# Performance work log

Measured on AMD Instinct MI355X. Metric: run time of the kernel, lower is better.

Reference implementation:

```python
import jax, jax.numpy as jnp
import numpy as np

B, F, V, E = 65536, 39, 100000, 16
EPS = 1e-5

def setup_inputs() -> dict:
    key = jax.random.key(0)
    ks = jax.random.split(key, 10)
    return {
        'Xi': jax.random.randint(ks[0], (B, F, 1), 0, V, dtype=jnp.int64) if jax.config.read('jax_enable_x64') else jax.random.randint(ks[0], (B, F, 1), 0, V, dtype=jnp.int32),
        'Xv': jax.random.uniform(ks[1], (B, F), dtype=jnp.float32),
        'emb1': jax.random.normal(ks[2], (F, V, 1), dtype=jnp.float32),
        'emb2': jax.random.normal(ks[3], (F, V, E), dtype=jnp.float32),
        'W1': jax.random.normal(ks[4], (F * E, 512), dtype=jnp.float32) * 0.02,
        'b1': jax.random.normal(ks[5], (512,), dtype=jnp.float32) * 0.02,
        'g1': jnp.ones((512,), jnp.float32),
        'be1': jnp.zeros((512,), jnp.float32),
        'W2': jax.random.normal(ks[6], (512, 256), dtype=jnp.float32) * 0.02,
        'b2': jax.random.normal(ks[7], (256,), dtype=jnp.float32) * 0.02,
        'g2': jnp.ones((256,), jnp.float32),
        'be2': jnp.zeros((256,), jnp.float32),
        'bias': jax.random.normal(ks[8], (1,), dtype=jnp.float32),
    }

def _batchnorm(x, g, b):
    mu = jnp.mean(x, axis=0)
    var = jnp.mean(jnp.square(x - mu), axis=0)  # biased var, torch BN training mode
    return (x - mu) * jax.lax.rsqrt(var + EPS) * g + b

def reference(Xi, Xv, emb1, emb2, W1, b1, g1, be1, W2, b2, g2, be2, bias):
    idx = Xi[:, :, 0]                                # [B, F]
    fidx = jnp.arange(F)[None, :]                    # [1, F]
    # fused per-field gathers: [B, F] and [B, F, E]
    first = emb1[fidx, idx, 0] * Xv                  # first-order, [B, F]
    fm2 = emb2[fidx, idx] * Xv[:, :, None]           # second-order embeds, [B, F, E]
    sum_emb = jnp.sum(fm2, axis=1)                   # [B, E]
    second = 0.5 * (jnp.square(sum_emb) - jnp.sum(jnp.square(fm2), axis=1))  # [B, E]
    # deep part (note: original forward never applies the final num_classes layer)
    deep = fm2.reshape(B, F * E)
    deep = _batchnorm(deep @ W1 + b1, g1, be1)
    deep = _batchnorm(deep @ W2 + b2, g2, be2)
    return bias + jnp.sum(first, axis=1) + jnp.sum(second, axis=1) + jnp.sum(deep, axis=1)
```

## Files before the change

kernel.cpp:

```cpp
#include <hip/hip_runtime.h>

#define B_ROWS 65536
#define F_FEAT 39
#define V_VOC  100000
#define D_PAD  640
#define BN_EPS 1e-5f
#define NPAIR  (39 * 32)

typedef __bf16 bf16x8 __attribute__((ext_vector_type(8)));
typedef float  f32x16 __attribute__((ext_vector_type(16)));

__device__ __forceinline__ unsigned short toBF(float x) {
  unsigned int u = __float_as_uint(x);
  u += 0x7fffu + ((u >> 16) & 1u);
  return (unsigned short)(u >> 16);
}

__global__ __launch_bounds__(256) void k0_prep(
    const int* __restrict__ Xi, const float* __restrict__ Xv,
    int* __restrict__ XiT, float* __restrict__ XvT,
    float* __restrict__ M, unsigned short* __restrict__ XT) {
  for (int i = threadIdx.x; i < 800; i += 256)
    M[(size_t)blockIdx.x * 800 + i] = 0.f;

  const int b0 = blockIdx.x * 128;
  for (int u = threadIdx.x; u < 16 * 128; u += 256) {
    int m = 624 + (u >> 7), j = u & 127;
    XT[(size_t)m * B_ROWS + b0 + j] = (m == 624) ? (unsigned short)0x3f80 : (unsigned short)0;
  }

  __shared__ int   ti[128][41];
  __shared__ float tv[128][41];
  for (int u = threadIdx.x; u < 128 * 39; u += 256) {
    int r = u / 39, f = u - r * 39;
    ti[r][f] = Xi[(size_t)b0 * 39 + u];
    tv[r][f] = Xv[(size_t)b0 * 39 + u];
  }
  __syncthreads();
  for (int u = threadIdx.x; u < 39 * 128; u += 256) {
    int f = u >> 7, j = u & 127;
    XiT[(size_t)f * B_ROWS + b0 + j] = ti[j][f];
    XvT[(size_t)f * B_ROWS + b0 + j] = tv[j][f];
  }
}

__global__ __launch_bounds__(1024) void k1f_gather(
    const int* __restrict__ XiT, const float* __restrict__ XvT,
    const float* __restrict__ emb1, const float* __restrict__ emb2,
    unsigned short* __restrict__ XT, float* __restrict__ FS1) {
  __shared__ unsigned short xs[2][16][264];

  const int seg = threadIdx.x & 3;
  const int bi  = threadIdx.x >> 2;
  const int dim = threadIdx.x >> 6;
  const int prt = threadIdx.x & 63;

  for (int idx = blockIdx.x; idx < NPAIR; idx += gridDim.x) {
    const int f = idx >> 5;
    const int c = idx & 31;
    const int b0 = c * 2048;
    const float* ef  = emb2 + (size_t)f * V_VOC * 16;
    const float* e1f = emb1 + (size_t)f * V_VOC;
    const int*   xi  = XiT + (size_t)f * B_ROWS + b0;
    const float* xv  = XvT + (size_t)f * B_ROWS + b0;
    unsigned short* xtBase = XT + (size_t)(f * 16) * B_ROWS + b0;
    float* fs1 = FS1 + (size_t)f * B_ROWS + b0;

    int   idA = xi[bi],        idB = xi[256 + bi];
    float xvA = xv[bi],        xvB = xv[256 + bi];
    float4 v = *reinterpret_cast<const float4*>(ef + (size_t)idA * 16 + seg * 4);

    for (int s = 0; s < 8; ++s) {
      const float4 cur = v;
      const float  xvc = xvA;
      const int    idc = idA;
      idA = idB; xvA = xvB;
      if (s + 2 < 8) {
        idB = xi[(s + 2) * 256 + bi];
        xvB = xv[(s + 2) * 256 + bi];
      }
      if (s + 1 < 8)
        v = *reinterpret_cast<const float4*>(ef + (size_t)idA * 16 + seg * 4);

      if (seg == 0) fs1[s * 256 + bi] = e1f[idc] * xvc;

      const int bf = s & 1;
      xs[bf][seg * 4 + 0][bi] = toBF(cur.x * xvc);
      xs[bf][seg * 4 + 1][bi] = toBF(cur.y * xvc);
      xs[bf][seg * 4 + 2][bi] = toBF(cur.z * xvc);
      xs[bf][seg * 4 + 3][bi] = toBF(cur.w * xvc);
      __syncthreads();
      uint2 w = *reinterpret_cast<const uint2*>(&xs[bf][dim][prt * 4]);
      *reinterpret_cast<uint2*>(xtBase + (size_t)dim * B_ROWS + s * 256 + prt * 4) = w;
    }
    __syncthreads();
  }
}

#define KSPLIT 64
__global__ __launch_bounds__(256) void k2_syrk(const unsigned short* __restrict__ XT,
                                               float* __restrict__ M) {
  const int p = blockIdx.x;
  const int xcd = p & 7;
  const int ks = ((p >> 3) / 15) * 8 + xcd;
  int pair = (p >> 3) % 15;
  int ti = 0;
  while (pair >= 5 - ti) { pair -= 5 - ti; ++ti; }
  const int tj = ti + pair;

  __shared__ unsigned short pa[128 * 64];
  __shared__ unsigned short pb[128 * 64];

  const int lane = threadIdx.x & 63, wid = threadIdx.x >> 6;
  const int wm = wid >> 1, wn = wid & 1;
  const int rl = lane & 31, hh = lane >> 5;

  f32x16 acc00, acc01, acc10, acc11;
#pragma unroll
  for (int i = 0; i < 16; ++i) { acc00[i] = 0.f; acc01[i] = 0.f; acc10[i] = 0.f; acc11[i] = 0.f; }

  const int krange = B_ROWS / KSPLIT;
  const int kbase = ks * krange;

  for (int kt = 0; kt < krange; kt += 64) {
    const int k0 = kbase + kt;
#pragma unroll
    for (int g2 = 0; g2 < 4; ++g2) {
      const int g = threadIdx.x + g2 * 256;
      const int r = g >> 3, j = g & 7;
      uint4 va = *reinterpret_cast<const uint4*>(XT + (size_t)(ti * 128 + r) * B_ROWS + k0 + j * 8);
      *reinterpret_cast<uint4*>((char*)pa + r * 128 + ((j ^ (r & 7)) << 4)) = va;
      uint4 vb = *reinterpret_cast<const uint4*>(XT + (size_t)(tj * 128 + r) * B_ROWS + k0 + j * 8);
      *reinterpret_cast<uint4*>((char*)pb + r * 128 + ((j ^ (r & 7)) << 4)) = vb;
    }
    __syncthreads();
#pragma unroll
    for (int kc = 0; kc < 4; ++kc) {
      const int ra0 = wm * 64 + rl, ra1 = wm * 64 + 32 + rl;
      const int rb0 = wn * 64 + rl, rb1 = wn * 64 + 32 + rl;
      bf16x8 a0 = *reinterpret_cast<const bf16x8*>((char*)pa + ra0 * 128 + (((kc * 2 + hh) ^ (ra0 & 7)) << 4));
      bf16x8 a1 = *reinterpret_cast<const bf16x8*>((char*)pa + ra1 * 128 + (((kc * 2 + hh) ^ (ra1 & 7)) << 4));
      bf16x8 b0 = *reinterpret_cast<const bf16x8*>((char*)pb + rb0 * 128 + (((kc * 2 + hh) ^ (rb0 & 7)) << 4));
      bf16x8 b1 = *reinterpret_cast<const bf16x8*>((char*)pb + rb1 * 128 + (((kc * 2 + hh) ^ (rb1 & 7)) << 4));
      acc00 = __builtin_amdgcn_mfma_f32_32x32x16_bf16(a0, b0, acc00, 0, 0, 0);
      acc01 = __builtin_amdgcn_mfma_f32_32x32x16_bf16(a0, b1, acc01, 0, 0, 0);
      acc10 = __builtin_amdgcn_mfma_f32_32x32x16_bf16(a1, b0, acc10, 0, 0, 0);
      acc11 = __builtin_amdgcn_mfma_f32_32x32x16_bf16(a1, b1, acc11, 0, 0, 0);
    }
    __syncthreads();
  }

#pragma unroll
  for (int rr = 0; rr < 16; ++rr) {
    const int rloc = (rr & 3) + ((rr >> 2) << 3) + hh * 4;
    const int row0 = ti * 128 + wm * 64 + rloc;
    const int row1 = row0 + 32;
    const int col0 = tj * 128 + wn * 64 + rl;
    atomicAdd(&M[row0 * D_PAD + col0], acc00[rr]);
    atomicAdd(&M[row0 * D_PAD + col0 + 32], acc01[rr]);
    atomicAdd(&M[row1 * D_PAD + col0], acc10[rr]);
    atomicAdd(&M[row1 * D_PAD + col0 + 32], acc11[rr]);
  }
}

__device__ __forceinline__ float fetchM(const float* M, int a, int b) {
  if ((a >> 7) > (b >> 7)) { int t = a; a = b; b = t; }
  return M[a * D_PAD + b];
}
__global__ void k3a_cov(const float* __restrict__ M, float* __restrict__ Cov,
                        float* __restrict__ mu) {
  const int i = blockIdx.x;
  const float inv = 1.f / 65536.f;
  const float mui = fetchM(M, 624, i) * inv;
  for (int j = threadIdx.x; j < D_PAD; j += 256) {
    float muj = fetchM(M, 624, j) * inv;
    Cov[i * D_PAD + j] = fetchM(M, i, j) * inv - mui * muj;
    if (i == 0) mu[j] = muj;
  }
}

__global__ __launch_bounds__(256) void qform(const float* __restrict__ Cov,
                                             const float* __restrict__ W, const int ldw,
                                             const float* __restrict__ g,
                                             float* __restrict__ alpha) {
  const int k0 = blockIdx.x * 2;
  __shared__ float w0s[624], w1s[624];
  for (int i = threadIdx.x; i < 624; i += 256) {
    w0s[i] = W[(size_t)i * ldw + k0];
    w1s[i] = W[(size_t)i * ldw + k0 + 1];
  }
  __syncthreads();
  const int j0 = threadIdx.x, j1 = threadIdx.x + 256, j2 = threadIdx.x + 512;
  const bool v2 = (j2 < 624);
  const float wj00 = w0s[j0], wj01 = w0s[j1], wj02 = v2 ? w0s[j2] : 0.f;
  const float wj10 = w1s[j0], wj11 = w1s[j1], wj12 = v2 ? w1s[j2] : 0.f;
  float acc0 = 0.f, acc1 = 0.f;
  for (int i = 0; i < 624; ++i) {
    const float wi0 = w0s[i], wi1 = w1s[i];
    const float* row = Cov + i * D_PAD;
    const float c0 = row[j0], c1 = row[j1], c2 = v2 ? row[j2] : 0.f;
    acc0 += wi0 * (c0 * wj00 + c1 * wj01 + c2 * wj02);
    acc1 += wi1 * (c0 * wj10 + c1 * wj11 + c2 * wj12);
  }
#pragma unroll
  for (int off = 32; off > 0; off >>= 1) {
    acc0 += __shfl_down(acc0, off);
    acc1 += __shfl_down(acc1, off);
  }
  __shared__ float pr[2][4];
  const int lane = threadIdx.x & 63, wv = threadIdx.x >> 6;
  if (lane == 0) { pr[0][wv] = acc0; pr[1][wv] = acc1; }
  __syncthreads();
  if (threadIdx.x == 0) {
    float v0 = pr[0][0] + pr[0][1] + pr[0][2] + pr[0][3];
    float v1 = pr[1][0] + pr[1][1] + pr[1][2] + pr[1][3];
    alpha[k0]     = g[k0]     * rsqrtf(v0 + BN_EPS);
    alpha[k0 + 1] = g[k0 + 1] * rsqrtf(v1 + BN_EPS);
  }
}

__global__ __launch_bounds__(256) void k3c_G(const float* __restrict__ W1,
                                             const float* __restrict__ alpha1,
                                             const float* __restrict__ W2,
                                             float* __restrict__ G) {
  const int i = blockIdx.x;
  __shared__ float a[512];
  for (int k = threadIdx.x; k < 512; k += 256)
    a[k] = W1[(size_t)i * 512 + k] * alpha1[k];
  __syncthreads();
  const int j = threadIdx.x;
  float acc = 0.f;
#pragma unroll 8
  for (int k = 0; k < 512; ++k) acc += a[k] * W2[(size_t)k * 256 + j];
  G[(size_t)i * 256 + j] = acc;
}

__global__ __launch_bounds__(256) void k3e_final(const float* __restrict__ G,
                                                 const float* __restrict__ alpha2,
                                                 const float* __restrict__ mu,
                                                 const float* __restrict__ be2,
                                                 const float* __restrict__ bias,
                                                 float* __restrict__ gw,
                                                 float* __restrict__ consts) {
  __shared__ float a2[256];
  __shared__ float gws[640];
  a2[threadIdx.x] = alpha2[threadIdx.x];
  __syncthreads();
  for (int i = threadIdx.x; i < 640; i += 256) {
    float acc = 0.f;
    if (i < 624) {
      const float* gr = G + (size_t)i * 256;
#pragma unroll 8
      for (int j = 0; j < 256; ++j) acc += gr[j] * a2[j];
    }
    gw[i] = acc;
    gws[i] = acc;
  }
  __syncthreads();
  float pm = 0.f;
  for (int i = threadIdx.x; i < 624; i += 256) pm += mu[i] * gws[i];
  float val = be2[threadIdx.x] - pm;
#pragma unroll
  for (int off = 32; off > 0; off >>= 1) val += __shfl_down(val, off);
  __shared__ float pr[4];
  const int lane = threadIdx.x & 63, wv = threadIdx.x >> 6;
  if (lane == 0) pr[wv] = val;
  __syncthreads();
  if (threadIdx.x == 0) consts[0] = bias[0] + pr[0] + pr[1] + pr[2] + pr[3];
}

__global__ __launch_bounds__(256) void k5_out(const float* __restrict__ FS1,
                                              const unsigned short* __restrict__ XT,
                                              const float* __restrict__ gw,
                                              const float* __restrict__ consts,
                                              float* __restrict__ out) {
  __shared__ float g[624];
  for (int m = threadIdx.x; m < 624; m += 256) g[m] = gw[m];
  __syncthreads();
  const int r = threadIdx.x >> 1, h = threadIdx.x & 1;
  const int b = blockIdx.x * 128 + r;
  const unsigned short* col = XT + b;

  float lin = 0.f, ssq = 0.f;
  float ps[16];
#pragma unroll
  for (int e = 0; e < 16; ++e) ps[e] = 0.f;

  const int m0 = h ? 320 : 0, m1 = h ? 624 : 320;
  for (int mo = m0; mo < m1; mo += 16) {
#pragma unroll
    for (int e = 0; e < 16; ++e) {
      const int m = mo + e;
      float x = __uint_as_float((unsigned int)col[(size_t)m * B_ROWS] << 16);
      lin += g[m] * x;
      ssq += x * x;
      ps[e] += x;
    }
  }
  const int fb = h ? 20 : 0, fe = h ? 39 : 20;
  for (int f = fb; f < fe; ++f)
    lin += FS1[(size_t)f * B_ROWS + b];

  float s2 = 0.f;
#pragma unroll
  for (int e = 0; e < 16; ++e) {
    float t = ps[e] + __shfl_xor(ps[e], 1);
    s2 += t * t;
  }
  float tot = lin + 0.5f * (0.5f * s2 - ssq);
  tot += __shfl_xor(tot, 1);
  if (h == 0) out[b] = tot + consts[0];
}

extern "C" void kernel_launch(void* const* d_in, const int* in_sizes, int n_in,
                              void* d_out, int out_size, void* d_ws, size_t ws_size,
                              hipStream_t stream) {
  const int*   Xi   = (const int*)d_in[0];
  const float* Xv   = (const float*)d_in[1];
  const float* emb1 = (const float*)d_in[2];
  const float* emb2 = (const float*)d_in[3];
  const float* W1   = (const float*)d_in[4];
  const float* g1   = (const float*)d_in[6];
  const float* W2   = (const float*)d_in[8];
  const float* g2   = (const float*)d_in[10];
  const float* be2  = (const float*)d_in[11];
  const float* bias = (const float*)d_in[12];
  float* out = (float*)d_out;
  char* ws = (char*)d_ws;

  const size_t OFF_XT  = 0;
  const size_t OFF_M   = OFF_XT + (size_t)640 * 65536 * 2;
  const size_t OFF_COV = OFF_M + (size_t)640 * 640 * 4;
  const size_t OFF_MU  = OFF_COV + (size_t)640 * 640 * 4;
  const size_t OFF_A1  = OFF_MU + 640 * 4;
  const size_t OFF_A2  = OFF_A1 + 512 * 4;
  const size_t OFF_G   = OFF_A2 + 256 * 4;
  const size_t OFF_GW  = OFF_G + (size_t)624 * 256 * 4;
  const size_t OFF_CN  = OFF_GW + 640 * 4;
  const size_t OFF_XIT = OFF_CN + 256;
  const size_t OFF_XVT = OFF_XIT + (size_t)39 * 65536 * 4;
  const size_t OFF_FS1 = OFF_XVT + (size_t)39 * 65536 * 4;

  unsigned short* XT = (unsigned short*)(ws + OFF_XT);
  float* M   = (float*)(ws + OFF_M);
  float* COV = (float*)(ws + OFF_COV);
  float* MU  = (float*)(ws + OFF_MU);
  float* A1  = (float*)(ws + OFF_A1);
  float* A2  = (float*)(ws + OFF_A2);
  float* G   = (float*)(ws + OFF_G);
  float* GW  = (float*)(ws + OFF_GW);
  float* CN  = (float*)(ws + OFF_CN);
  int*   XIT = (int*)(ws + OFF_XIT);
  float* XVT = (float*)(ws + OFF_XVT);
  float* FS1 = (float*)(ws + OFF_FS1);

  k0_prep<<<512, 256, 0, stream>>>(Xi, Xv, XIT, XVT, M, XT);
  k1f_gather<<<256, 1024, 0, stream>>>(XIT, XVT, emb1, emb2, XT, FS1);
  k2_syrk<<<15 * KSPLIT, 256, 0, stream>>>(XT, M);
  k3a_cov<<<640, 256, 0, stream>>>(M, COV, MU);
  qform<<<256, 256, 0, stream>>>(COV, W1, 512, g1, A1);
  k3c_G<<<624, 256, 0, stream>>>(W1, A1, W2, G);
  qform<<<128, 256, 0, stream>>>(COV, G, 256, g2, A2);
  k3e_final<<<1, 256, 0, stream>>>(G, A2, MU, be2, bias, GW, CN);
  k5_out<<<512, 256, 0, stream>>>(FS1, XT, GW, CN, out);
}
```

Measured before the change: 370.6 us.

## Bucket-sort indices by vocab row before embedding gather for locality

Replaces the single fused gather with a counting-sort pipeline: histogram indices per field into 256-row buckets, prefix-sum the counts, scatter (id, batch, value) into bucket order, gather embeddings in that sorted order writing row-major bf16, then transpose into the feature-major XT layout. The goal is more coalesced, cache-friendly reads from the embedding table. It adds several kernel launches and extra global traffic for the sorted arrays and the intermediate XB buffer. The scattered 32-byte writes in the gather may lose coalescing. KSPLIT for the syrk kernel also drops from 64 to 32.

```diff
diff --git a/kernel.cpp b/kernel.cpp
--- a/kernel.cpp
+++ b/kernel.cpp
@@ -5,7 +5,9 @@
 #define V_VOC  100000
 #define D_PAD  640
 #define BN_EPS 1e-5f
-#define NPAIR  (39 * 32)
+#define NB     391
+#define SUBS   8
+#define SUBSZ  8192
 
 typedef __bf16 bf16x8 __attribute__((ext_vector_type(8)));
 typedef float  f32x16 __attribute__((ext_vector_type(16)));
@@ -44,60 +46,135 @@
   }
 }
 
-__global__ __launch_bounds__(1024) void k1f_gather(
+__global__ __launch_bounds__(256) void k_hist(const int* __restrict__ XiT,
+                                              unsigned int* __restrict__ HIST) {
+  const int f = blockIdx.x / SUBS, sub = blockIdx.x % SUBS;
+  __shared__ unsigned int h[NB];
+  for (int j = threadIdx.x; j < NB; j += 256) h[j] = 0;
+  __syncthreads();
+  const int* xi = XiT + (size_t)f * B_ROWS + sub * SUBSZ;
+  for (int it = 0; it < SUBSZ / 256; ++it)
+    atomicAdd(&h[(unsigned)xi[it * 256 + threadIdx.x] >> 8], 1u);
+  __syncthreads();
+  unsigned int* out = HIST + (size_t)blockIdx.x * NB;
+  for (int j = threadIdx.x; j < NB; j += 256) out[j] = h[j];
+}
+
+__global__ __launch_bounds__(512) void k_prefix(const unsigned int* __restrict__ HIST,
+                                                unsigned int* __restrict__ SOFF) {
+  const int f = blockIdx.x;
+  const int t = threadIdx.x;
+  __shared__ unsigned int sa[512];
+  __shared__ unsigned int tot[NB];
+  unsigned int mytot = 0;
+  if (t < NB) {
+    for (int s = 0; s < SUBS; ++s) mytot += HIST[((size_t)f * SUBS + s) * NB + t];
+    tot[t] = mytot;
+  }
+  sa[t] = (t < NB) ? mytot : 0;
+  __syncthreads();
+  for (int off = 1; off < 512; off <<= 1) {
+    unsigned int v = sa[t];
+    if (t >= off) v += sa[t - off];
+    __syncthreads();
+    sa[t] = v;
+    __syncthreads();
+  }
+  if (t < NB) {
+    unsigned int running = sa[t] - tot[t];
+    for (int s = 0; s < SUBS; ++s) {
+      SOFF[((size_t)f * SUBS + s) * NB + t] = running;
+      running += HIST[((size_t)f * SUBS + s) * NB + t];
+    }
+  }
+}
+
+__global__ __launch_bounds__(256) void k_scatter(
     const int* __restrict__ XiT, const float* __restrict__ XvT,
-    const float* __restrict__ emb1, const float* __restrict__ emb2,
-    unsigned short* __restrict__ XT, float* __restrict__ FS1) {
-  __shared__ unsigned short xs[2][16][264];
-
-  const int seg = threadIdx.x & 3;
-  const int bi  = threadIdx.x >> 2;
-  const int dim = threadIdx.x >> 6;
-  const int prt = threadIdx.x & 63;
-
-  for (int idx = blockIdx.x; idx < NPAIR; idx += gridDim.x) {
-    const int f = idx >> 5;
-    const int c = idx & 31;
-    const int b0 = c * 2048;
-    const float* ef  = emb2 + (size_t)f * V_VOC * 16;
-    const float* e1f = emb1 + (size_t)f * V_VOC;
-    const int*   xi  = XiT + (size_t)f * B_ROWS + b0;
-    const float* xv  = XvT + (size_t)f * B_ROWS + b0;
-    unsigned short* xtBase = XT + (size_t)(f * 16) * B_ROWS + b0;
-    float* fs1 = FS1 + (size_t)f * B_ROWS + b0;
-
-    int   idA = xi[bi],        idB = xi[256 + bi];
-    float xvA = xv[bi],        xvB = xv[256 + bi];
-    float4 v = *reinterpret_cast<const float4*>(ef + (size_t)idA * 16 + seg * 4);
-
-    for (int s = 0; s < 8; ++s) {
-      const float4 cur = v;
-      const float  xvc = xvA;
-      const int    idc = idA;
-      idA = idB; xvA = xvB;
-      if (s + 2 < 8) {
-        idB = xi[(s + 2) * 256 + bi];
-        xvB = xv[(s + 2) * 256 + bi];
-      }
-      if (s + 1 < 8)
-        v = *reinterpret_cast<const float4*>(ef + (size_t)idA * 16 + seg * 4);
-
-      if (seg == 0) fs1[s * 256 + bi] = e1f[idc] * xvc;
-
-      const int bf = s & 1;
-      xs[bf][seg * 4 + 0][bi] = toBF(cur.x * xvc);
-      xs[bf][seg * 4 + 1][bi] = toBF(cur.y * xvc);
-      xs[bf][seg * 4 + 2][bi] = toBF(cur.z * xvc);
-      xs[bf][seg * 4 + 3][bi] = toBF(cur.w * xvc);
-      __syncthreads();
-      uint2 w = *reinterpret_cast<const uint2*>(&xs[bf][dim][prt * 4]);
-      *reinterpret_cast<uint2*>(xtBase + (size_t)dim * B_ROWS + s * 256 + prt * 4) = w;
-    }
-    __syncthreads();
-  }
-}
-
-#define KSPLIT 64
+    const unsigned int* __restrict__ SOFF,
+    unsigned int* __restrict__ EID, unsigned int* __restrict__ EB,
+    float* __restrict__ EV) {
+  const int f = blockIdx.x / SUBS, sub = blockIdx.x % SUBS;
+  __shared__ unsigned int cur[NB];
+  for (int j = threadIdx.x; j < NB; j += 256)
+    cur[j] = SOFF[(size_t)blockIdx.x * NB + j];
+  __syncthreads();
+  const int base = sub * SUBSZ;
+  for (int it = 0; it < SUBSZ / 256; ++it) {
+    const int b = base + it * 256 + threadIdx.x;
+    const unsigned int id = (unsigned)XiT[(size_t)f * B_ROWS + b];
+    const float xv = XvT[(size_t)f * B_ROWS + b];
+    const unsigned int pos = atomicAdd(&cur[id >> 8], 1u);
+    const size_t g = (size_t)f * B_ROWS + pos;
+    EID[g] = id;
+    EB[g]  = (unsigned)b;
+    EV[g]  = xv;
+  }
+}
+
+__global__ __launch_bounds__(256) void k_gather(
+    const unsigned int* __restrict__ EID, const unsigned int* __restrict__ EB,
+    const float* __restrict__ EV, const float* __restrict__ emb1,
+    const float* __restrict__ emb2,
+    unsigned short* __restrict__ XB, float* __restrict__ FS1) {
+  const int f = blockIdx.x >> 5;
+  const int c = blockIdx.x & 31;
+  const size_t ebase = (size_t)f * B_ROWS + c * 2048;
+  const float* ef  = emb2 + (size_t)f * V_VOC * 16;
+  const float* e1f = emb1 + (size_t)f * V_VOC;
+
+  for (int it = 0; it < 8; ++it) {
+    const size_t e = ebase + it * 256 + threadIdx.x;
+    const unsigned int id = EID[e];
+    const unsigned int b  = EB[e];
+    const float xv = EV[e];
+    const float4* er = reinterpret_cast<const float4*>(ef + (size_t)id * 16);
+    float4 q0 = er[0], q1 = er[1], q2 = er[2], q3 = er[3];
+    unsigned int w[8];
+    w[0] = (unsigned)toBF(q0.x * xv) | ((unsigned)toBF(q0.y * xv) << 16);
+    w[1] = (unsigned)toBF(q0.z * xv) | ((unsigned)toBF(q0.w * xv) << 16);
+    w[2] = (unsigned)toBF(q1.x * xv) | ((unsigned)toBF(q1.y * xv) << 16);
+    w[3] = (unsigned)toBF(q1.z * xv) | ((unsigned)toBF(q1.w * xv) << 16);
+    w[4] = (unsigned)toBF(q2.x * xv) | ((unsigned)toBF(q2.y * xv) << 16);
+    w[5] = (unsigned)toBF(q2.z * xv) | ((unsigned)toBF(q2.w * xv) << 16);
+    w[6] = (unsigned)toBF(q3.x * xv) | ((unsigned)toBF(q3.y * xv) << 16);
+    w[7] = (unsigned)toBF(q3.z * xv) | ((unsigned)toBF(q3.w * xv) << 16);
+    uint4* dst = reinterpret_cast<uint4*>(XB + ((size_t)f * B_ROWS + b) * 16);
+    uint4 d0; d0.x = w[0]; d0.y = w[1]; d0.z = w[2]; d0.w = w[3];
+    uint4 d1; d1.x = w[4]; d1.y = w[5]; d1.z = w[6]; d1.w = w[7];
+    dst[0] = d0; dst[1] = d1;
+    FS1[(size_t)f * B_ROWS + b] = e1f[id] * xv;
+  }
+}
+
+__global__ __launch_bounds__(256) void k_transpose(const unsigned short* __restrict__ XB,
+                                                   unsigned short* __restrict__ XT) {
+  const int f = blockIdx.y;
+  const int b0 = blockIdx.x * 512;
+  __shared__ unsigned int ls[16][257];
+  const int t = threadIdx.x;
+  const int bb = b0 + 2 * t;
+  const uint4* s0 = reinterpret_cast<const uint4*>(XB + ((size_t)f * B_ROWS + bb) * 16);
+  uint4 qa0 = s0[0], qa1 = s0[1], qb0 = s0[2], qb1 = s0[3];
+  const unsigned short* pa0 = reinterpret_cast<const unsigned short*>(&qa0);
+  const unsigned short* pa1 = reinterpret_cast<const unsigned short*>(&qa1);
+  const unsigned short* pb0 = reinterpret_cast<const unsigned short*>(&qb0);
+  const unsigned short* pb1 = reinterpret_cast<const unsigned short*>(&qb1);
+#pragma unroll
+  for (int d = 0; d < 8; ++d) {
+    ls[d][t]     = (unsigned)pa0[d] | ((unsigned)pb0[d] << 16);
+    ls[d + 8][t] = (unsigned)pa1[d] | ((unsigned)pb1[d] << 16);
+  }
+  __syncthreads();
+#pragma unroll
+  for (int d = 0; d < 16; ++d) {
+    unsigned int* row = reinterpret_cast<unsigned int*>(
+        XT + (size_t)(f * 16 + d) * B_ROWS + b0);
+    row[t] = ls[d][t];
+  }
+}
+
+#define KSPLIT 32
 __global__ __launch_bounds__(256) void k2_syrk(const unsigned short* __restrict__ XT,
                                                float* __restrict__ M) {
   const int p = blockIdx.x;
@@ -328,36 +405,39 @@
   float* out = (float*)d_out;
   char* ws = (char*)d_ws;
 
-  const size_t OFF_XT  = 0;
-  const size_t OFF_M   = OFF_XT + (size_t)640 * 65536 * 2;
-  const size_t OFF_COV = OFF_M + (size_t)640 * 640 * 4;
-  const size_t OFF_MU  = OFF_COV + (size_t)640 * 640 * 4;
-  const size_t OFF_A1  = OFF_MU + 640 * 4;
-  const size_t OFF_A2  = OFF_A1 + 512 * 4;
-  const size_t OFF_G   = OFF_A2 + 256 * 4;
-  const size_t OFF_GW  = OFF_G + (size_t)624 * 256 * 4;
-  const size_t OFF_CN  = OFF_GW + 640 * 4;
-  const size_t OFF_XIT = OFF_CN + 256;
-  const size_t OFF_XVT = OFF_XIT + (size_t)39 * 65536 * 4;
-  const size_t OFF_FS1 = OFF_XVT + (size_t)39 * 65536 * 4;
-
-  unsigned short* XT = (unsigned short*)(ws + OFF_XT);
-  float* M   = (float*)(ws + OFF_M);
-  float* COV = (float*)(ws + OFF_COV);
-  float* MU  = (float*)(ws + OFF_MU);
-  float* A1  = (float*)(ws + OFF_A1);
-  float* A2  = (float*)(ws + OFF_A2);
-  float* G   = (float*)(ws + OFF_G);
-  float* GW  = (float*)(ws + OFF_GW);
-  float* CN  = (float*)(ws + OFF_CN);
-  int*   XIT = (int*)(ws + OFF_XIT);
-  float* XVT = (float*)(ws + OFF_XVT);
-  float* FS1 = (float*)(ws + OFF_FS1);
+  const size_t SZ_XT  = (size_t)D_PAD * B_ROWS * 2;
+  const size_t SZ_XB  = (size_t)F_FEAT * B_ROWS * 32;
+  const size_t SZ_FB  = (size_t)F_FEAT * B_ROWS * 4;
+  const size_t SZ_HS  = (size_t)F_FEAT * SUBS * NB * 4;
+
+  size_t off = 0;
+  unsigned short* XT = (unsigned short*)(ws + off); off += SZ_XT;
+  unsigned short* XB = (unsigned short*)(ws + off); off += SZ_XB;
+  float* M    = (float*)(ws + off); off += (size_t)D_PAD * D_PAD * 4;
+  float* COV  = (float*)(ws + off); off += (size_t)D_PAD * D_PAD * 4;
+  float* MU   = (float*)(ws + off); off += D_PAD * 4;
+  float* A1   = (float*)(ws + off); off += 512 * 4;
+  float* A2   = (float*)(ws + off); off += 256 * 4;
+  float* G    = (float*)(ws + off); off += (size_t)624 * 256 * 4;
+  float* GW   = (float*)(ws + off); off += D_PAD * 4;
+  float* CN   = (float*)(ws + off); off += 256;
+  int*   XIT  = (int*)(ws + off);   off += SZ_FB;
+  float* XVT  = (float*)(ws + off); off += SZ_FB;
+  float* FS1  = (float*)(ws + off); off += SZ_FB;
+  unsigned int* EID = (unsigned int*)(ws + off); off += SZ_FB;
+  unsigned int* EB  = (unsigned int*)(ws + off); off += SZ_FB;
+  float*        EV  = (float*)(ws + off);        off += SZ_FB;
+  unsigned int* HIST = (unsigned int*)(ws + off); off += SZ_HS;
+  unsigned int* SOFF = (unsigned int*)(ws + off); off += SZ_HS;
 
   k0_prep<<<512, 256, 0, stream>>>(Xi, Xv, XIT, XVT, M, XT);
-  k1f_gather<<<256, 1024, 0, stream>>>(XIT, XVT, emb1, emb2, XT, FS1);
+  k_hist<<<F_FEAT * SUBS, 256, 0, stream>>>(XIT, HIST);
+  k_prefix<<<F_FEAT, 512, 0, stream>>>(HIST, SOFF);
+  k_scatter<<<F_FEAT * SUBS, 256, 0, stream>>>(XIT, XVT, SOFF, EID, EB, EV);
+  k_gather<<<F_FEAT * 32, 256, 0, stream>>>(EID, EB, EV, emb1, emb2, XB, FS1);
+  k_transpose<<<dim3(128, F_FEAT), 256, 0, stream>>>(XB, XT);
   k2_syrk<<<15 * KSPLIT, 256, 0, stream>>>(XT, M);
-  k3a_cov<<<640, 256, 0, stream>>>(M, COV, MU);
+  k3a_cov<<<D_PAD, 256, 0, stream>>>(M, COV, MU);
   qform<<<256, 256, 0, stream>>>(COV, W1, 512, g1, A1);
   k3c_G<<<624, 256, 0, stream>>>(W1, A1, W2, G);
   qform<<<128, 256, 0, stream>>>(COV, G, 256, g2, A2);
```

After: 511.8 us. 1.38x slower.
